# Performance work log

Hardware: AMD Instinct MI355X
Metric: run time of the kernel (lower is better)

The kernel has to match this reference:

```python
import jax, jax.numpy as jnp
import numpy as np

NUM_HEADS = 32
NUM_KV_HEADS = 8
HEAD_DIM = 128
HIDDEN = 4096
ROPE_THETA = 10000.0
SLIDING_WINDOW = 1024
NEG_INF = -1e9


def _make_sliding_window_mask(q_len, kv_len, window):
    # additive mask: 0 where attendable (causal AND within window), -inf otherwise
    i = jnp.arange(q_len)[:, None]
    j = jnp.arange(kv_len)[None, :]
    allowed = (j <= i) & (j > i - window)
    return jnp.where(allowed, 0.0, NEG_INF).astype(jnp.float32)[None, None]  # [1,1,q,kv]


def _rope_tables(seq_len, head_dim, theta):
    inv_freq = 1.0 / (theta ** (jnp.arange(0, head_dim, 2, dtype=jnp.float32) / head_dim))
    t = jnp.arange(seq_len, dtype=jnp.float32)
    freqs = jnp.einsum('i,j->ij', t, inv_freq)        # [S, D/2]
    emb = jnp.concatenate([freqs, freqs], axis=-1)     # [S, D]
    return jnp.cos(emb), jnp.sin(emb)


def _rotate_half(x):
    d = x.shape[-1] // 2
    return jnp.concatenate([-x[..., d:], x[..., :d]], axis=-1)


def setup_inputs() -> dict:
    key = jax.random.key(0)
    ks = jax.random.split(key, 5)
    B, S = 1, 2048
    sc = 0.02
    hidden_states = jax.random.normal(ks[0], (B, S, HIDDEN), dtype=jnp.float32)
    Wq = jax.random.normal(ks[1], (HIDDEN, NUM_HEADS * HEAD_DIM), dtype=jnp.float32) * sc
    Wk = jax.random.normal(ks[2], (HIDDEN, NUM_KV_HEADS * HEAD_DIM), dtype=jnp.float32) * sc
    Wv = jax.random.normal(ks[3], (HIDDEN, NUM_KV_HEADS * HEAD_DIM), dtype=jnp.float32) * sc
    Wo = jax.random.normal(ks[4], (NUM_HEADS * HEAD_DIM, HIDDEN), dtype=jnp.float32) * sc
    attention_mask = _make_sliding_window_mask(S, S, SLIDING_WINDOW)
    position_ids = jnp.arange(S, dtype=jnp.int64)[None, :]
    return {"hidden_states": hidden_states, "attention_mask": attention_mask,
            "position_ids": position_ids, "Wq": Wq, "Wk": Wk, "Wv": Wv, "Wo": Wo}


def reference(hidden_states, attention_mask, position_ids, Wq, Wk, Wv, Wo):
    B, S, _ = hidden_states.shape
    # projections
    q = (hidden_states @ Wq).reshape(B, S, NUM_HEADS, HEAD_DIM).transpose(0, 2, 1, 3)      # [B,H,S,D]
    k = (hidden_states @ Wk).reshape(B, S, NUM_KV_HEADS, HEAD_DIM).transpose(0, 2, 1, 3)   # [B,Hk,S,D]
    v = (hidden_states @ Wv).reshape(B, S, NUM_KV_HEADS, HEAD_DIM).transpose(0, 2, 1, 3)
    # RoPE
    cos_t, sin_t = _rope_tables(S, HEAD_DIM, ROPE_THETA)
    cos = cos_t[position_ids][:, None]  # [B,1,S,D]
    sin = sin_t[position_ids][:, None]
    q = q * cos + _rotate_half(q) * sin
    k = k * cos + _rotate_half(k) * sin
    # repeat_kv (GQA): [B,Hk,S,D] -> [B,H,S,D]
    n_rep = NUM_HEADS // NUM_KV_HEADS
    k = jnp.repeat(k, n_rep, axis=1)
    v = jnp.repeat(v, n_rep, axis=1)
    # attention
    scores = jnp.einsum('bhqd,bhkd->bhqk', q, k) / np.sqrt(HEAD_DIM)
    scores = scores + attention_mask
    probs = jax.nn.softmax(scores, axis=-1)
    out = jnp.einsum('bhqk,bhkd->bhqd', probs, v)
    out = out.transpose(0, 2, 1, 3).reshape(B, S, HIDDEN)
    return out @ Wo
```

## Files before the change

### kernel.cpp

```cpp
#include <hip/hip_runtime.h>

typedef __attribute__((ext_vector_type(8))) short short8;
typedef __attribute__((ext_vector_type(4))) short s16x4;
typedef __attribute__((ext_vector_type(4))) float f32x4;
typedef unsigned short u16;
typedef unsigned int u32;

__device__ __forceinline__ u16 f2bf(float f) {
  union { float f; unsigned int u; } v; v.f = f;
  unsigned int r = (v.u + 0x7FFFu + ((v.u >> 16) & 1u)) >> 16;
  return (u16)r;
}
__device__ __forceinline__ float bf2f(u16 b) {
  union { unsigned int u; float f; } v; v.u = ((unsigned int)b) << 16;
  return v.f;
}
__device__ __forceinline__ void load_lds16(const void* g, void* l) {
  __builtin_amdgcn_global_load_lds((const __attribute__((address_space(1))) void*)g,
                                   (__attribute__((address_space(3))) void*)l, 16, 0, 0);
}

__global__ void cvt_f32_bf16_kernel(const float* __restrict__ in, u16* __restrict__ out, int n4) {
  int i = blockIdx.x * blockDim.x + threadIdx.x;
  if (i >= n4) return;
  float4 v = ((const float4*)in)[i];
  ushort4 o;
  o.x = f2bf(v.x); o.y = f2bf(v.y); o.z = f2bf(v.z); o.w = f2bf(v.w);
  ((ushort4*)out)[i] = o;
}

__global__ void combine2_f32_kernel(float* __restrict__ out, const u16* __restrict__ p0,
                                    const u16* __restrict__ p1, int n8) {
  int i = blockIdx.x * blockDim.x + threadIdx.x;
  if (i >= n8) return;
  short8 a = ((const short8*)p0)[i];
  short8 b = ((const short8*)p1)[i];
  float4 o0, o1;
  o0.x = bf2f((u16)a[0]) + bf2f((u16)b[0]);
  o0.y = bf2f((u16)a[1]) + bf2f((u16)b[1]);
  o0.z = bf2f((u16)a[2]) + bf2f((u16)b[2]);
  o0.w = bf2f((u16)a[3]) + bf2f((u16)b[3]);
  o1.x = bf2f((u16)a[4]) + bf2f((u16)b[4]);
  o1.y = bf2f((u16)a[5]) + bf2f((u16)b[5]);
  o1.z = bf2f((u16)a[6]) + bf2f((u16)b[6]);
  o1.w = bf2f((u16)a[7]) + bf2f((u16)b[7]);
  ((float4*)out)[i * 2]     = o0;
  ((float4*)out)[i * 2 + 1] = o1;
}

__global__ void combine_kv_kernel(const u16* __restrict__ PKV, u16* __restrict__ Kb,
                                  u16* __restrict__ Vt) {
  int i = blockIdx.x * blockDim.x + threadIdx.x;
  const u16* src; u16* dst; size_t off;
  if (i < 262144) { off = (size_t)i; dst = Kb; src = PKV; }
  else            { off = (size_t)(i - 262144); dst = Vt; src = PKV + 2097152; }
  float s[8] = {0.f, 0.f, 0.f, 0.f, 0.f, 0.f, 0.f, 0.f};
#pragma unroll
  for (int z = 0; z < 4; ++z) {
    short8 v = *(const short8*)(src + (size_t)z * 4194304 + off * 8);
#pragma unroll
    for (int j = 0; j < 8; ++j) s[j] += bf2f((u16)v[j]);
  }
  short8 o;
#pragma unroll
  for (int j = 0; j < 8; ++j) o[j] = (short)f2bf(s[j]);
  ((short8*)dst)[off] = o;
}

__device__ __forceinline__ void tconv64_tile(const float* __restrict__ W, u16* __restrict__ Wt,
                                             int K, int N, int nb, int kb, int tid) {
  __shared__ float tile[64][65];
  int tx = tid & 15, ty = tid >> 4;
  const float* src = W + (size_t)(kb + ty) * N + nb + tx * 4;
#pragma unroll
  for (int i = 0; i < 4; ++i) {
    float4 v = *(const float4*)(src + (size_t)i * 16 * N);
    tile[ty + i * 16][tx * 4 + 0] = v.x;
    tile[ty + i * 16][tx * 4 + 1] = v.y;
    tile[ty + i * 16][tx * 4 + 2] = v.z;
    tile[ty + i * 16][tx * 4 + 3] = v.w;
  }
  __syncthreads();
  u16* dst = Wt + (size_t)(nb + ty) * K + kb + tx * 4;
#pragma unroll
  for (int i = 0; i < 4; ++i) {
    s16x4 o;
#pragma unroll
    for (int j = 0; j < 4; ++j) o[j] = (short)f2bf(tile[tx * 4 + j][ty + i * 16]);
    *(s16x4*)(dst + (size_t)i * 16 * K) = o;
  }
}

__global__ void tconv3_kernel(const float* __restrict__ Wq, const float* __restrict__ Wk,
                              const float* __restrict__ Wv, u16* __restrict__ WqT,
                              u16* __restrict__ WkvT) {
  int id = blockIdx.x;
  if (id < 4096)      tconv64_tile(Wq, WqT, 4096, 4096, (id & 63) * 64, (id >> 6) * 64, threadIdx.x);
  else if (id < 5120) { int t = id - 4096; tconv64_tile(Wk, WkvT, 4096, 1024, (t & 15) * 64, (t >> 4) * 64, threadIdx.x); }
  else                { int t = id - 5120; tconv64_tile(Wv, WkvT + (size_t)1024 * 4096, 4096, 1024, (t & 15) * 64, (t >> 4) * 64, threadIdx.x); }
}

__global__ void tconv1_kernel(const float* __restrict__ W, u16* __restrict__ Wt) {
  int id = blockIdx.x;
  tconv64_tile(W, Wt, 4096, 4096, (id & 63) * 64, (id >> 6) * 64, threadIdx.x);
}

__global__ void rope_kernel(u16* __restrict__ Qb, const u16* __restrict__ Qp1, u16* __restrict__ Kb) {
  int idx = blockIdx.x * blockDim.x + threadIdx.x;
  int j, t, hh, s;
  if (idx < 4194304) {
    j = idx & 63; t = idx >> 6; hh = t & 31; s = t >> 5;
    float invf = exp2f(-(float)j * (13.287712379549449f / 64.0f));
    float ang = (float)s * invf;
    float sn, cs;
    sincosf(ang, &sn, &cs);
    size_t base = (size_t)s * 4096 + hh * 128 + j;
    u16* p = Qb + base;
    const u16* p1 = Qp1 + base;
    float a = bf2f(p[0]) + bf2f(p1[0]);
    float b = bf2f(p[64]) + bf2f(p1[64]);
    const float scale = 0.12751781828987514f;
    p[0]  = f2bf((a * cs - b * sn) * scale);
    p[64] = f2bf((b * cs + a * sn) * scale);
  } else {
    int id = idx - 4194304;
    j = id & 63; t = id >> 6; hh = t & 7; s = t >> 3;
    float invf = exp2f(-(float)j * (13.287712379549449f / 64.0f));
    float ang = (float)s * invf;
    float sn, cs;
    sincosf(ang, &sn, &cs);
    u16* p = Kb + (size_t)s * 1024 + hh * 128 + j;
    float a = bf2f(p[0]), b = bf2f(p[64]);
    p[0]  = f2bf(a * cs - b * sn);
    p[64] = f2bf(b * cs + a * sn);
  }
}

__global__ __launch_bounds__(512, 1) void gemm256_kernel(
    const u16* __restrict__ A, const u16* __restrict__ B,
    u16* __restrict__ C0, u16* __restrict__ C1, int N, int K, int KH) {
  __shared__ u16 As[2][256 * 64];
  __shared__ u16 Bs[2][256 * 64];
  int tid = threadIdx.x, lane = tid & 63, wid = tid >> 6;
  int wr = wid >> 2, wc = wid & 3;
  int g = lane >> 4, q = lane & 15;
  int id = blockIdx.z * gridDim.x * gridDim.y + blockIdx.y * gridDim.x + blockIdx.x;
  int tot = gridDim.x * gridDim.y * gridDim.z;
  int swz = (id & 7) * (tot >> 3) + (id >> 3);
  int perh = gridDim.x * gridDim.y;
  int z = swz / perh, rem = swz % perh;
  int m0 = (rem / gridDim.x) * 256, n0 = (rem % gridDim.x) * 256;
  int k0 = z * KH;
  f32x4 acc[8][4];
#pragma unroll
  for (int i = 0; i < 8; ++i)
#pragma unroll
    for (int j = 0; j < 4; ++j) acc[i][j] = (f32x4){0.f, 0.f, 0.f, 0.f};
  int srow = tid >> 3;
  int scol = ((tid & 7) ^ (srow & 7)) << 3;
  const u16* ga = A + (size_t)(m0 + srow) * K + k0 + scol;
  const u16* gb = B + (size_t)(n0 + srow) * K + k0 + scol;
  int xorm = (q & 7) << 3;
  int arow = wr * 128 + q;
  int brow = wc * 64 + q;
  int nt = KH >> 6;

  auto stage = [&](int buf, int t) {
    const u16* pa = ga + t * 64;
    const u16* pb = gb + t * 64;
#pragma unroll
    for (int it = 0; it < 4; ++it) {
      load_lds16(pa + (size_t)it * 64 * K, (char*)(&As[buf][0]) + it * 8192 + tid * 16);
      load_lds16(pb + (size_t)it * 64 * K, (char*)(&Bs[buf][0]) + it * 8192 + tid * 16);
    }
  };

  stage(0, 0);
  stage(1, 1);
  asm volatile("s_waitcnt vmcnt(8)" ::: "memory");
  __builtin_amdgcn_s_barrier();
  for (int t = 0; t < nt; ++t) {
    int cur = t & 1;
    int col0 = (g * 8) ^ xorm;
    short8 a0[8], b0[4];
#pragma unroll
    for (int m = 0; m < 8; ++m) a0[m] = *(const short8*)&As[cur][(arow + m * 16) * 64 + col0];
#pragma unroll
    for (int n = 0; n < 4; ++n) b0[n] = *(const short8*)&Bs[cur][(brow + n * 16) * 64 + col0];
    __builtin_amdgcn_s_setprio(1);
#pragma unroll
    for (int m = 0; m < 8; ++m)
#pragma unroll
      for (int n = 0; n < 4; ++n)
        acc[m][n] = __builtin_amdgcn_mfma_f32_16x16x32_bf16(a0[m], b0[n], acc[m][n], 0, 0, 0);
    __builtin_amdgcn_s_setprio(0);
    int col1 = (32 + g * 8) ^ xorm;
    short8 a1[8], b1[4];
#pragma unroll
    for (int m = 0; m < 8; ++m) a1[m] = *(const short8*)&As[cur][(arow + m * 16) * 64 + col1];
#pragma unroll
    for (int n = 0; n < 4; ++n) b1[n] = *(const short8*)&Bs[cur][(brow + n * 16) * 64 + col1];
    asm volatile("s_waitcnt lgkmcnt(0)" ::: "memory");
    __builtin_amdgcn_s_barrier();
    if (t + 2 < nt) stage(cur, t + 2);
    __builtin_amdgcn_sched_barrier(0);
    __builtin_amdgcn_s_setprio(1);
#pragma unroll
    for (int m = 0; m < 8; ++m)
#pragma unroll
      for (int n = 0; n < 4; ++n)
        acc[m][n] = __builtin_amdgcn_mfma_f32_16x16x32_bf16(a1[m], b1[n], acc[m][n], 0, 0, 0);
    __builtin_amdgcn_s_setprio(0);
    if (t + 2 < nt)      { asm volatile("s_waitcnt vmcnt(8)" ::: "memory"); }
    else if (t + 1 < nt) { asm volatile("s_waitcnt vmcnt(0)" ::: "memory"); }
    __builtin_amdgcn_s_barrier();
  }
  int crow = m0 + wr * 128 + g * 4;
  int ccol = n0 + wc * 64 + q;
  u16* dst = z ? C1 : C0;
#pragma unroll
  for (int fm = 0; fm < 8; ++fm)
#pragma unroll
    for (int fn = 0; fn < 4; ++fn)
#pragma unroll
      for (int r = 0; r < 4; ++r)
        dst[(size_t)(crow + fm * 16 + r) * N + ccol + fn * 16] = f2bf(acc[fm][fn][r]);
}

__global__ __launch_bounds__(512, 1) void gemm_kv256_kernel(
    const u16* __restrict__ A, const u16* __restrict__ B,
    u16* __restrict__ PKV, int K, int KH) {
  __shared__ u16 As[2][256 * 64];
  __shared__ u16 Bs[2][256 * 64];
  int tid = threadIdx.x, lane = tid & 63, wid = tid >> 6;
  int wr = wid >> 2, wc = wid & 3;
  int g = lane >> 4, q = lane & 15;
  int id = blockIdx.z * 64 + blockIdx.y * 8 + blockIdx.x;
  int swz = (id & 7) * 32 + (id >> 3);
  int z = swz >> 6, rem = swz & 63;
  int m0 = (rem >> 3) * 256, n0 = (rem & 7) * 256;
  int k0 = z * KH;
  f32x4 acc[8][4];
#pragma unroll
  for (int i = 0; i < 8; ++i)
#pragma unroll
    for (int j = 0; j < 4; ++j) acc[i][j] = (f32x4){0.f, 0.f, 0.f, 0.f};
  int srow = tid >> 3;
  int scol = ((tid & 7) ^ (srow & 7)) << 3;
  const u16* ga = A + (size_t)(m0 + srow) * K + k0 + scol;
  const u16* gb = B + (size_t)(n0 + srow) * K + k0 + scol;
  int xorm = (q & 7) << 3;
  int arow = wr * 128 + q;
  int brow = wc * 64 + q;
  int nt = KH >> 6;

  auto stage = [&](int buf, int t) {
    const u16* pa = ga + t * 64;
    const u16* pb = gb + t * 64;
#pragma unroll
    for (int it = 0; it < 4; ++it) {
      load_lds16(pa + (size_t)it * 64 * K, (char*)(&As[buf][0]) + it * 8192 + tid * 16);
      load_lds16(pb + (size_t)it * 64 * K, (char*)(&Bs[buf][0]) + it * 8192 + tid * 16);
    }
  };

  stage(0, 0);
  stage(1, 1);
  asm volatile("s_waitcnt vmcnt(8)" ::: "memory");
  __builtin_amdgcn_s_barrier();
  for (int t = 0; t < nt; ++t) {
    int cur = t & 1;
    int col0 = (g * 8) ^ xorm;
    short8 a0[8], b0[4];
#pragma unroll
    for (int m = 0; m < 8; ++m) a0[m] = *(const short8*)&As[cur][(arow + m * 16) * 64 + col0];
#pragma unroll
    for (int n = 0; n < 4; ++n) b0[n] = *(const short8*)&Bs[cur][(brow + n * 16) * 64 + col0];
    __builtin_amdgcn_s_setprio(1);
#pragma unroll
    for (int m = 0; m < 8; ++m)
#pragma unroll
      for (int n = 0; n < 4; ++n)
        acc[m][n] = __builtin_amdgcn_mfma_f32_16x16x32_bf16(a0[m], b0[n], acc[m][n], 0, 0, 0);
    __builtin_amdgcn_s_setprio(0);
    int col1 = (32 + g * 8) ^ xorm;
    short8 a1[8], b1[4];
#pragma unroll
    for (int m = 0; m < 8; ++m) a1[m] = *(const short8*)&As[cur][(arow + m * 16) * 64 + col1];
#pragma unroll
    for (int n = 0; n < 4; ++n) b1[n] = *(const short8*)&Bs[cur][(brow + n * 16) * 64 + col1];
    asm volatile("s_waitcnt lgkmcnt(0)" ::: "memory");
    __builtin_amdgcn_s_barrier();
    if (t + 2 < nt) stage(cur, t + 2);
    __builtin_amdgcn_sched_barrier(0);
    __builtin_amdgcn_s_setprio(1);
#pragma unroll
    for (int m = 0; m < 8; ++m)
#pragma unroll
      for (int n = 0; n < 4; ++n)
        acc[m][n] = __builtin_amdgcn_mfma_f32_16x16x32_bf16(a1[m], b1[n], acc[m][n], 0, 0, 0);
    __builtin_amdgcn_s_setprio(0);
    if (t + 2 < nt)      { asm volatile("s_waitcnt vmcnt(8)" ::: "memory"); }
    else if (t + 1 < nt) { asm volatile("s_waitcnt vmcnt(0)" ::: "memory"); }
    __builtin_amdgcn_s_barrier();
  }
  int crow = m0 + wr * 128 + g * 4;
  int ccol = n0 + wc * 64 + q;
  u16* Kpart = PKV + (size_t)z * 4194304;
  u16* Vpart = Kpart + 2097152;
  if (n0 < 1024) {
#pragma unroll
    for (int fm = 0; fm < 8; ++fm)
#pragma unroll
      for (int fn = 0; fn < 4; ++fn)
#pragma unroll
        for (int r = 0; r < 4; ++r)
          Kpart[(size_t)(crow + fm * 16 + r) * 1024 + ccol + fn * 16] = f2bf(acc[fm][fn][r]);
  } else {
#pragma unroll
    for (int fn = 0; fn < 4; ++fn) {
      int vcol = ccol + fn * 16 - 1024;
#pragma unroll
      for (int fm = 0; fm < 8; ++fm) {
        s16x4 o;
#pragma unroll
        for (int r = 0; r < 4; ++r) o[r] = (short)f2bf(acc[fm][fn][r]);
        *(s16x4*)(Vpart + (size_t)vcol * 2048 + crow + fm * 16) = o;
      }
    }
  }
}

__global__ __launch_bounds__(512, 4) void attn_kernel(
    const u16* __restrict__ Q, const u16* __restrict__ Kg,
    const u16* __restrict__ Vt, u16* __restrict__ O) {
  __shared__ u16 Ks[2][64 * 128];
  __shared__ u16 Vs[2][128 * 64];
  int tid = threadIdx.x, lane = tid & 63, w = tid >> 6;
  int wg = w >> 2;
  int g = lane >> 4, q = lane & 15;
  int q0 = blockIdx.x * 128;
  int h = blockIdx.y, hk = h >> 2;
  int qbase = q0 + wg * 64;
  int qrow = qbase + (w & 3) * 16;
  int xorm = (lane & 7) << 3;
  short8 qf[4];
  {
    const u16* qp = Q + (size_t)(qrow + q) * 4096 + h * 128 + g * 8;
#pragma unroll
    for (int kk = 0; kk < 4; ++kk) qf[kk] = *(const short8*)(qp + kk * 32);
  }
  float mrow = -1e30f, lsum = 0.f;
  f32x4 of[8];
#pragma unroll
  for (int d = 0; d < 8; ++d) of[d] = (f32x4){0.f, 0.f, 0.f, 0.f};
  int bjt_lo = (q0 >= 1024) ? ((q0 - 1023) >> 6) : 0;
  int bjt_hi = (q0 + 64) >> 6;
  int wjt_lo = (qbase >= 1024) ? ((qbase - 1023) >> 6) : 0;
  int wjt_hi = qbase >> 6;
  int krow = tid >> 4;
  int kchunk = (tid & 15) ^ (krow & 7);
  const u16* kbase = Kg + (size_t)krow * 1024 + hk * 128 + (kchunk << 3);
  int vrow = tid >> 3;
  int vchunk = (tid & 7) ^ (vrow & 7);
  const u16* vbase = Vt + (size_t)(hk * 128 + vrow) * 2048 + (vchunk << 3);

  auto stageK = [&](int buf, int j0) {
    const u16* gp = kbase + (size_t)j0 * 1024;
#pragma unroll
    for (int it = 0; it < 2; ++it)
      load_lds16(gp + (size_t)it * 32 * 1024, (char*)(&Ks[buf][0]) + it * 8192 + tid * 16);
  };
  auto stageV = [&](int buf, int j0) {
    const u16* gp = vbase + j0;
#pragma unroll
    for (int it = 0; it < 2; ++it)
      load_lds16(gp + (size_t)it * 64 * 2048, (char*)(&Vs[buf][0]) + it * 8192 + tid * 16);
  };

  int cur = 0;
  stageK(0, bjt_lo << 6);
  stageV(0, bjt_lo << 6);
  asm volatile("s_waitcnt vmcnt(0)" ::: "memory");
  __syncthreads();
  for (int jt = bjt_lo; jt <= bjt_hi; ++jt) {
    int j0 = jt << 6;
    if (jt < bjt_hi) { stageK(cur ^ 1, j0 + 64); stageV(cur ^ 1, j0 + 64); }
    if (jt >= wjt_lo && jt <= wjt_hi) {
      f32x4 sf[4];
#pragma unroll
      for (int nt = 0; nt < 4; ++nt) sf[nt] = (f32x4){0.f, 0.f, 0.f, 0.f};
      const u16* ks = &Ks[cur][0];
      __builtin_amdgcn_s_setprio(1);
#pragma unroll
      for (int kk = 0; kk < 4; ++kk) {
        short8 qv = qf[kk];
        int col = (kk * 32 + g * 8) ^ xorm;
#pragma unroll
        for (int nt = 0; nt < 4; ++nt) {
          short8 kf = *(const short8*)&ks[(nt * 16 + q) * 128 + col];
          sf[nt] = __builtin_amdgcn_mfma_f32_16x16x32_bf16(kf, qv, sf[nt], 0, 0, 0);
        }
      }
      __builtin_amdgcn_s_setprio(0);
      float p[4][4];
#pragma unroll
      for (int nt = 0; nt < 4; ++nt)
#pragma unroll
        for (int r = 0; r < 4; ++r) p[nt][r] = sf[nt][r];
      if (j0 + 63 > qrow || j0 + 1009 <= qrow) {
        int qq = qrow + q;
        int kb = j0 + g * 4;
#pragma unroll
        for (int nt = 0; nt < 4; ++nt)
#pragma unroll
          for (int r = 0; r < 4; ++r) {
            int key = kb + nt * 16 + r;
            if (key > qq || key + 1024 <= qq) p[nt][r] = -1e9f;
          }
      }
      float tm = p[0][0];
#pragma unroll
      for (int nt = 0; nt < 4; ++nt)
#pragma unroll
        for (int r = 0; r < 4; ++r) tm = fmaxf(tm, p[nt][r]);
      tm = fmaxf(tm, __shfl_xor(tm, 16));
      tm = fmaxf(tm, __shfl_xor(tm, 32));
      if (__any(tm > mrow + 8.f)) {
        float nm = fmaxf(mrow, tm);
        float sc = __builtin_amdgcn_exp2f(mrow - nm);
        mrow = nm;
        lsum *= sc;
#pragma unroll
        for (int d = 0; d < 8; ++d) of[d] *= sc;
      }
      float ps = 0.f;
#pragma unroll
      for (int nt = 0; nt < 4; ++nt)
#pragma unroll
        for (int r = 0; r < 4; ++r) {
          float e = __builtin_amdgcn_exp2f(p[nt][r] - mrow);
          p[nt][r] = e;
          ps += e;
        }
      ps += __shfl_xor(ps, 16);
      ps += __shfl_xor(ps, 32);
      lsum += ps;
      u32 pk[4][2];
#pragma unroll
      for (int nt = 0; nt < 4; ++nt) {
        pk[nt][0] = __builtin_amdgcn_perm(__float_as_uint(p[nt][1]), __float_as_uint(p[nt][0]), 0x07060302u);
        pk[nt][1] = __builtin_amdgcn_perm(__float_as_uint(p[nt][3]), __float_as_uint(p[nt][2]), 0x07060302u);
      }
      int s0 = q + ((g & 1) ? 32 : 0);
      int s1 = s0 + 16;
      bool hi_sel = g >= 2;
      const u16* vs = &Vs[cur][0];
      __builtin_amdgcn_s_setprio(1);
#pragma unroll
      for (int kh = 0; kh < 2; ++kh) {
        int lo = kh * 2, hi = lo + 1;
        u32 a0 = (u32)__shfl((int)pk[lo][0], s0);
        u32 a1 = (u32)__shfl((int)pk[lo][1], s0);
        u32 b0 = (u32)__shfl((int)pk[hi][0], s0);
        u32 b1 = (u32)__shfl((int)pk[hi][1], s0);
        u32 a2 = (u32)__shfl((int)pk[lo][0], s1);
        u32 a3 = (u32)__shfl((int)pk[lo][1], s1);
        u32 b2 = (u32)__shfl((int)pk[hi][0], s1);
        u32 b3 = (u32)__shfl((int)pk[hi][1], s1);
        union { u32 u[4]; short8 s; } pb;
        pb.u[0] = hi_sel ? b0 : a0;
        pb.u[1] = hi_sel ? b1 : a1;
        pb.u[2] = hi_sel ? b2 : a2;
        pb.u[3] = hi_sel ? b3 : a3;
        int col = (kh * 32 + g * 8) ^ xorm;
#pragma unroll
        for (int dt = 0; dt < 8; ++dt) {
          short8 vv = *(const short8*)&vs[(dt * 16 + q) * 64 + col];
          of[dt] = __builtin_amdgcn_mfma_f32_16x16x32_bf16(vv, pb.s, of[dt], 0, 0, 0);
        }
      }
      __builtin_amdgcn_s_setprio(0);
    }
    asm volatile("s_waitcnt vmcnt(0)" ::: "memory");
    __builtin_amdgcn_s_barrier();
    cur ^= 1;
  }
  float inv = 1.f / lsum;
  u16* op = O + (size_t)(qrow + q) * 4096 + h * 128 + g * 4;
#pragma unroll
  for (int dt = 0; dt < 8; ++dt) {
    s16x4 o4;
#pragma unroll
    for (int r = 0; r < 4; ++r) o4[r] = (short)f2bf(of[dt][r] * inv);
    *(s16x4*)(op + dt * 16) = o4;
  }
}

extern "C" void kernel_launch(void* const* d_in, const int* in_sizes, int n_in,
                              void* d_out, int out_size, void* d_ws, size_t ws_size,
                              hipStream_t stream) {
  (void)in_sizes; (void)n_in; (void)out_size;
  const float* hs = (const float*)d_in[0];
  const float* Wq = (const float*)d_in[3];
  const float* Wk = (const float*)d_in[4];
  const float* Wv = (const float*)d_in[5];
  const float* Wo = (const float*)d_in[6];
  float* out = (float*)d_out;
  char* ws = (char*)d_ws;

  u16* Xb   = (u16*)(ws + 0);
  u16* Wt   = (u16*)(ws + 16777216);
  u16* WkvT = (u16*)(ws + 50331648);
  u16* Qb   = (u16*)(ws + 67108864);
  u16* Kb   = (u16*)(ws + 83886080);
  u16* Vtb  = (u16*)(ws + 88080384);
  u16* Ab   = (u16*)(ws + 96468992);
  u16* P1q  = Ab;
  u16* PKV  = Wt;
  u16* P0o  = WkvT;
  u16* P1o  = Qb;
  if (ws_size < 113246208u) return;

  cvt_f32_bf16_kernel<<<dim3(2097152 / 256), 256, 0, stream>>>(hs, Xb, 2097152);

  tconv3_kernel<<<dim3(6144), 256, 0, stream>>>(Wq, Wk, Wv, Wt, WkvT);

  gemm256_kernel<<<dim3(16, 8, 2), 512, 0, stream>>>(Xb, Wt, Qb, P1q, 4096, 4096, 2048);

  gemm_kv256_kernel<<<dim3(8, 8, 4), 512, 0, stream>>>(Xb, WkvT, PKV, 4096, 1024);
  combine_kv_kernel<<<dim3(2048), 256, 0, stream>>>(PKV, Kb, Vtb);

  rope_kernel<<<dim3(20480), 256, 0, stream>>>(Qb, P1q, Kb);

  attn_kernel<<<dim3(16, 32), 512, 0, stream>>>(Qb, Kb, Vtb, Ab);

  tconv1_kernel<<<dim3(4096), 256, 0, stream>>>(Wo, Wt);
  gemm256_kernel<<<dim3(16, 8, 2), 512, 0, stream>>>(Ab, Wt, P0o, P1o, 4096, 4096, 2048);
  combine2_f32_kernel<<<dim3(4096), 256, 0, stream>>>(out, P0o, P1o, 1048576);
}
```

Measured before the change: 311.7 us.

## Restructure GEMM mainloop into eight-phase half-tile pipeline with finer staging

Replaces the two-phase double-buffered GEMM loop with an eight-phase schedule that splits each 64-wide K tile into two 32-wide halves per matrix, interleaving global-to-LDS loads of the half tiles with smaller MFMA groups separated by barriers. The Q/O and KV GEMMs are unified into one templated kernel with an epilogue switch. The aim is to overlap memory traffic with compute more finely and cut register pressure by holding only 4 A fragments at a time. In exchange it adds more barriers per tile and drops the XOR swizzle, so the 64-byte-stride LDS reads may hit bank conflicts.

```diff
diff --git a/kernel.cpp b/kernel.cpp
--- a/kernel.cpp
+++ b/kernel.cpp
@@ -136,11 +136,11 @@
   }
 }
 
-__global__ __launch_bounds__(512, 1) void gemm256_kernel(
+template<int KVEPI>
+__global__ __launch_bounds__(512, 1) void gemm8p_kernel(
     const u16* __restrict__ A, const u16* __restrict__ B,
     u16* __restrict__ C0, u16* __restrict__ C1, int N, int K, int KH) {
-  __shared__ u16 As[2][256 * 64];
-  __shared__ u16 Bs[2][256 * 64];
+  __shared__ u16 Sh[2][2][2][8192];
   int tid = threadIdx.x, lane = tid & 63, wid = tid >> 6;
   int wr = wid >> 2, wc = wid & 3;
   int g = lane >> 4, q = lane & 15;
@@ -156,178 +156,120 @@
   for (int i = 0; i < 8; ++i)
 #pragma unroll
     for (int j = 0; j < 4; ++j) acc[i][j] = (f32x4){0.f, 0.f, 0.f, 0.f};
-  int srow = tid >> 3;
-  int scol = ((tid & 7) ^ (srow & 7)) << 3;
+  int srow = tid >> 2;
+  int scol = (tid & 3) * 8;
   const u16* ga = A + (size_t)(m0 + srow) * K + k0 + scol;
   const u16* gb = B + (size_t)(n0 + srow) * K + k0 + scol;
-  int xorm = (q & 7) << 3;
   int arow = wr * 128 + q;
   int brow = wc * 64 + q;
   int nt = KH >> 6;
 
-  auto stage = [&](int buf, int t) {
-    const u16* pa = ga + t * 64;
-    const u16* pb = gb + t * 64;
-#pragma unroll
-    for (int it = 0; it < 4; ++it) {
-      load_lds16(pa + (size_t)it * 64 * K, (char*)(&As[buf][0]) + it * 8192 + tid * 16);
-      load_lds16(pb + (size_t)it * 64 * K, (char*)(&Bs[buf][0]) + it * 8192 + tid * 16);
-    }
+  auto stageH = [&](int b, int mat, int h, int t) {
+    const u16* gp = (mat ? gb : ga) + t * 64 + h * 32;
+    char* dst = (char*)&Sh[b][mat][h][0];
+#pragma unroll
+    for (int it = 0; it < 2; ++it)
+      load_lds16(gp + (size_t)it * 128 * K, dst + it * 8192 + tid * 16);
   };
-
-  stage(0, 0);
-  stage(1, 1);
-  asm volatile("s_waitcnt vmcnt(8)" ::: "memory");
+  auto readA = [&](int b, int h, int fb, short8 (&af)[4]) {
+    const u16* s = &Sh[b][0][h][0];
+#pragma unroll
+    for (int m = 0; m < 4; ++m)
+      af[m] = *(const short8*)&s[(arow + (fb + m) * 16) * 32 + g * 8];
+  };
+  auto readB = [&](int b, int h, short8 (&bf)[4]) {
+    const u16* s = &Sh[b][1][h][0];
+#pragma unroll
+    for (int n = 0; n < 4; ++n)
+      bf[n] = *(const short8*)&s[(brow + n * 16) * 32 + g * 8];
+  };
+
+  stageH(0, 0, 0, 0); stageH(0, 1, 0, 0);
+  stageH(0, 0, 1, 0); stageH(0, 1, 1, 0);
+  stageH(1, 0, 0, 1); stageH(1, 1, 0, 1);
+  asm volatile("s_waitcnt vmcnt(4)" ::: "memory");
   __builtin_amdgcn_s_barrier();
-  for (int t = 0; t < nt; ++t) {
-    int cur = t & 1;
-    int col0 = (g * 8) ^ xorm;
-    short8 a0[8], b0[4];
-#pragma unroll
-    for (int m = 0; m < 8; ++m) a0[m] = *(const short8*)&As[cur][(arow + m * 16) * 64 + col0];
-#pragma unroll
-    for (int n = 0; n < 4; ++n) b0[n] = *(const short8*)&Bs[cur][(brow + n * 16) * 64 + col0];
-    __builtin_amdgcn_s_setprio(1);
-#pragma unroll
-    for (int m = 0; m < 8; ++m)
-#pragma unroll
-      for (int n = 0; n < 4; ++n)
-        acc[m][n] = __builtin_amdgcn_mfma_f32_16x16x32_bf16(a0[m], b0[n], acc[m][n], 0, 0, 0);
-    __builtin_amdgcn_s_setprio(0);
-    int col1 = (32 + g * 8) ^ xorm;
-    short8 a1[8], b1[4];
-#pragma unroll
-    for (int m = 0; m < 8; ++m) a1[m] = *(const short8*)&As[cur][(arow + m * 16) * 64 + col1];
-#pragma unroll
-    for (int n = 0; n < 4; ++n) b1[n] = *(const short8*)&Bs[cur][(brow + n * 16) * 64 + col1];
-    asm volatile("s_waitcnt lgkmcnt(0)" ::: "memory");
-    __builtin_amdgcn_s_barrier();
-    if (t + 2 < nt) stage(cur, t + 2);
-    __builtin_amdgcn_sched_barrier(0);
-    __builtin_amdgcn_s_setprio(1);
-#pragma unroll
-    for (int m = 0; m < 8; ++m)
-#pragma unroll
-      for (int n = 0; n < 4; ++n)
-        acc[m][n] = __builtin_amdgcn_mfma_f32_16x16x32_bf16(a1[m], b1[n], acc[m][n], 0, 0, 0);
-    __builtin_amdgcn_s_setprio(0);
-    if (t + 2 < nt)      { asm volatile("s_waitcnt vmcnt(8)" ::: "memory"); }
-    else if (t + 1 < nt) { asm volatile("s_waitcnt vmcnt(0)" ::: "memory"); }
-    __builtin_amdgcn_s_barrier();
-  }
+
+#define PHASE(FB)                                                        \
+  __builtin_amdgcn_s_barrier();                                          \
+  asm volatile("s_waitcnt lgkmcnt(0)" ::: "memory");                     \
+  __builtin_amdgcn_sched_barrier(0);                                     \
+  __builtin_amdgcn_s_setprio(1);                                         \
+  _Pragma("unroll")                                                      \
+  for (int m = 0; m < 4; ++m)                                            \
+    _Pragma("unroll")                                                    \
+    for (int n = 0; n < 4; ++n)                                          \
+      acc[FB + m][n] = __builtin_amdgcn_mfma_f32_16x16x32_bf16(          \
+          af[m], bf[n], acc[FB + m][n], 0, 0, 0);                        \
+  __builtin_amdgcn_s_setprio(0);                                         \
+  __builtin_amdgcn_s_barrier();
+
+  for (int t = 0; t < nt; t += 2) {
+    bool s2 = (t + 2 < nt);
+    short8 af[4], bf[4];
+    readA(0, 0, 0, af); readB(0, 0, bf);
+    stageH(1, 0, 1, t + 1);
+    PHASE(0)
+    readA(0, 0, 4, af);
+    stageH(1, 1, 1, t + 1);
+    PHASE(4)
+    readA(0, 1, 0, af); readB(0, 1, bf);
+    if (s2) stageH(0, 0, 0, t + 2);
+    PHASE(0)
+    readA(0, 1, 4, af);
+    if (s2) stageH(0, 1, 0, t + 2);
+    PHASE(4)
+    readA(1, 0, 0, af); readB(1, 0, bf);
+    if (s2) { stageH(0, 0, 1, t + 2); asm volatile("s_waitcnt vmcnt(6)" ::: "memory"); }
+    else    { asm volatile("s_waitcnt vmcnt(0)" ::: "memory"); }
+    PHASE(0)
+    readA(1, 0, 4, af);
+    if (s2) stageH(0, 1, 1, t + 2);
+    PHASE(4)
+    readA(1, 1, 0, af); readB(1, 1, bf);
+    if (s2) stageH(1, 0, 0, t + 3);
+    PHASE(0)
+    readA(1, 1, 4, af);
+    if (s2) { stageH(1, 1, 0, t + 3); asm volatile("s_waitcnt vmcnt(4)" ::: "memory"); }
+    PHASE(4)
+  }
+#undef PHASE
+
   int crow = m0 + wr * 128 + g * 4;
   int ccol = n0 + wc * 64 + q;
-  u16* dst = z ? C1 : C0;
-#pragma unroll
-  for (int fm = 0; fm < 8; ++fm)
-#pragma unroll
-    for (int fn = 0; fn < 4; ++fn)
-#pragma unroll
-      for (int r = 0; r < 4; ++r)
-        dst[(size_t)(crow + fm * 16 + r) * N + ccol + fn * 16] = f2bf(acc[fm][fn][r]);
-}
-
-__global__ __launch_bounds__(512, 1) void gemm_kv256_kernel(
-    const u16* __restrict__ A, const u16* __restrict__ B,
-    u16* __restrict__ PKV, int K, int KH) {
-  __shared__ u16 As[2][256 * 64];
-  __shared__ u16 Bs[2][256 * 64];
-  int tid = threadIdx.x, lane = tid & 63, wid = tid >> 6;
-  int wr = wid >> 2, wc = wid & 3;
-  int g = lane >> 4, q = lane & 15;
-  int id = blockIdx.z * 64 + blockIdx.y * 8 + blockIdx.x;
-  int swz = (id & 7) * 32 + (id >> 3);
-  int z = swz >> 6, rem = swz & 63;
-  int m0 = (rem >> 3) * 256, n0 = (rem & 7) * 256;
-  int k0 = z * KH;
-  f32x4 acc[8][4];
-#pragma unroll
-  for (int i = 0; i < 8; ++i)
-#pragma unroll
-    for (int j = 0; j < 4; ++j) acc[i][j] = (f32x4){0.f, 0.f, 0.f, 0.f};
-  int srow = tid >> 3;
-  int scol = ((tid & 7) ^ (srow & 7)) << 3;
-  const u16* ga = A + (size_t)(m0 + srow) * K + k0 + scol;
-  const u16* gb = B + (size_t)(n0 + srow) * K + k0 + scol;
-  int xorm = (q & 7) << 3;
-  int arow = wr * 128 + q;
-  int brow = wc * 64 + q;
-  int nt = KH >> 6;
-
-  auto stage = [&](int buf, int t) {
-    const u16* pa = ga + t * 64;
-    const u16* pb = gb + t * 64;
-#pragma unroll
-    for (int it = 0; it < 4; ++it) {
-      load_lds16(pa + (size_t)it * 64 * K, (char*)(&As[buf][0]) + it * 8192 + tid * 16);
-      load_lds16(pb + (size_t)it * 64 * K, (char*)(&Bs[buf][0]) + it * 8192 + tid * 16);
+  if (KVEPI) {
+    u16* Kpart = C0 + (size_t)z * 4194304;
+    u16* Vpart = Kpart + 2097152;
+    if (n0 < 1024) {
+#pragma unroll
+      for (int fm = 0; fm < 8; ++fm)
+#pragma unroll
+        for (int fn = 0; fn < 4; ++fn)
+#pragma unroll
+          for (int r = 0; r < 4; ++r)
+            Kpart[(size_t)(crow + fm * 16 + r) * 1024 + ccol + fn * 16] = f2bf(acc[fm][fn][r]);
+    } else {
+#pragma unroll
+      for (int fn = 0; fn < 4; ++fn) {
+        int vcol = ccol + fn * 16 - 1024;
+#pragma unroll
+        for (int fm = 0; fm < 8; ++fm) {
+          s16x4 o;
+#pragma unroll
+          for (int r = 0; r < 4; ++r) o[r] = (short)f2bf(acc[fm][fn][r]);
+          *(s16x4*)(Vpart + (size_t)vcol * 2048 + crow + fm * 16) = o;
+        }
+      }
     }
-  };
-
-  stage(0, 0);
-  stage(1, 1);
-  asm volatile("s_waitcnt vmcnt(8)" ::: "memory");
-  __builtin_amdgcn_s_barrier();
-  for (int t = 0; t < nt; ++t) {
-    int cur = t & 1;
-    int col0 = (g * 8) ^ xorm;
-    short8 a0[8], b0[4];
-#pragma unroll
-    for (int m = 0; m < 8; ++m) a0[m] = *(const short8*)&As[cur][(arow + m * 16) * 64 + col0];
-#pragma unroll
-    for (int n = 0; n < 4; ++n) b0[n] = *(const short8*)&Bs[cur][(brow + n * 16) * 64 + col0];
-    __builtin_amdgcn_s_setprio(1);
-#pragma unroll
-    for (int m = 0; m < 8; ++m)
-#pragma unroll
-      for (int n = 0; n < 4; ++n)
-        acc[m][n] = __builtin_amdgcn_mfma_f32_16x16x32_bf16(a0[m], b0[n], acc[m][n], 0, 0, 0);
-    __builtin_amdgcn_s_setprio(0);
-    int col1 = (32 + g * 8) ^ xorm;
-    short8 a1[8], b1[4];
-#pragma unroll
-    for (int m = 0; m < 8; ++m) a1[m] = *(const short8*)&As[cur][(arow + m * 16) * 64 + col1];
-#pragma unroll
-    for (int n = 0; n < 4; ++n) b1[n] = *(const short8*)&Bs[cur][(brow + n * 16) * 64 + col1];
-    asm volatile("s_waitcnt lgkmcnt(0)" ::: "memory");
-    __builtin_amdgcn_s_barrier();
-    if (t + 2 < nt) stage(cur, t + 2);
-    __builtin_amdgcn_sched_barrier(0);
-    __builtin_amdgcn_s_setprio(1);
-#pragma unroll
-    for (int m = 0; m < 8; ++m)
-#pragma unroll
-      for (int n = 0; n < 4; ++n)
-        acc[m][n] = __builtin_amdgcn_mfma_f32_16x16x32_bf16(a1[m], b1[n], acc[m][n], 0, 0, 0);
-    __builtin_amdgcn_s_setprio(0);
-    if (t + 2 < nt)      { asm volatile("s_waitcnt vmcnt(8)" ::: "memory"); }
-    else if (t + 1 < nt) { asm volatile("s_waitcnt vmcnt(0)" ::: "memory"); }
-    __builtin_amdgcn_s_barrier();
-  }
-  int crow = m0 + wr * 128 + g * 4;
-  int ccol = n0 + wc * 64 + q;
-  u16* Kpart = PKV + (size_t)z * 4194304;
-  u16* Vpart = Kpart + 2097152;
-  if (n0 < 1024) {
+  } else {
+    u16* dst = z ? C1 : C0;
 #pragma unroll
     for (int fm = 0; fm < 8; ++fm)
 #pragma unroll
       for (int fn = 0; fn < 4; ++fn)
 #pragma unroll
         for (int r = 0; r < 4; ++r)
-          Kpart[(size_t)(crow + fm * 16 + r) * 1024 + ccol + fn * 16] = f2bf(acc[fm][fn][r]);
-  } else {
-#pragma unroll
-    for (int fn = 0; fn < 4; ++fn) {
-      int vcol = ccol + fn * 16 - 1024;
-#pragma unroll
-      for (int fm = 0; fm < 8; ++fm) {
-        s16x4 o;
-#pragma unroll
-        for (int r = 0; r < 4; ++r) o[r] = (short)f2bf(acc[fm][fn][r]);
-        *(s16x4*)(Vpart + (size_t)vcol * 2048 + crow + fm * 16) = o;
-      }
-    }
+          dst[(size_t)(crow + fm * 16 + r) * N + ccol + fn * 16] = f2bf(acc[fm][fn][r]);
   }
 }
 
@@ -526,9 +468,9 @@
 
   tconv3_kernel<<<dim3(6144), 256, 0, stream>>>(Wq, Wk, Wv, Wt, WkvT);
 
-  gemm256_kernel<<<dim3(16, 8, 2), 512, 0, stream>>>(Xb, Wt, Qb, P1q, 4096, 4096, 2048);
-
-  gemm_kv256_kernel<<<dim3(8, 8, 4), 512, 0, stream>>>(Xb, WkvT, PKV, 4096, 1024);
+  gemm8p_kernel<0><<<dim3(16, 8, 2), 512, 0, stream>>>(Xb, Wt, Qb, P1q, 4096, 4096, 2048);
+
+  gemm8p_kernel<1><<<dim3(8, 8, 4), 512, 0, stream>>>(Xb, WkvT, PKV, nullptr, 2048, 4096, 1024);
   combine_kv_kernel<<<dim3(2048), 256, 0, stream>>>(PKV, Kb, Vtb);
 
   rope_kernel<<<dim3(20480), 256, 0, stream>>>(Qb, P1q, Kb);
@@ -536,6 +478,6 @@
   attn_kernel<<<dim3(16, 32), 512, 0, stream>>>(Qb, Kb, Vtb, Ab);
 
   tconv1_kernel<<<dim3(4096), 256, 0, stream>>>(Wo, Wt);
-  gemm256_kernel<<<dim3(16, 8, 2), 512, 0, stream>>>(Ab, Wt, P0o, P1o, 4096, 4096, 2048);
+  gemm8p_kernel<0><<<dim3(16, 8, 2), 512, 0, stream>>>(Ab, Wt, P0o, P1o, 4096, 4096, 2048);
   combine2_f32_kernel<<<dim3(4096), 256, 0, stream>>>(out, P0o, P1o, 1048576);
 }
```

Result: slower. 326.6 us (+4.8%).

## Fuse RoPE into KV combine and attention Q load, drop rope kernel

Applied to the files above, without the earlier changes.

Removes the standalone RoPE kernel. K rotation now happens inside the split-K combine kernel, and Q's two split-K partials are summed, rotated and scaled when the attention kernel loads Q fragments. This saves one full read-modify-write pass over Q and K plus a launch. The cost is that attention reads two Q buffers and does sincos work per block, and the attention output buffer is moved onto Xb.

```diff
diff --git a/kernel.cpp b/kernel.cpp
--- a/kernel.cpp
+++ b/kernel.cpp
@@ -48,23 +48,48 @@
   ((float4*)out)[i * 2 + 1] = o1;
 }
 
-__global__ void combine_kv_kernel(const u16* __restrict__ PKV, u16* __restrict__ Kb,
-                                  u16* __restrict__ Vt) {
+__global__ void combine_kv_rope_kernel(const u16* __restrict__ PKV, u16* __restrict__ Kb,
+                                       u16* __restrict__ Vt) {
   int i = blockIdx.x * blockDim.x + threadIdx.x;
-  const u16* src; u16* dst; size_t off;
-  if (i < 262144) { off = (size_t)i; dst = Kb; src = PKV; }
-  else            { off = (size_t)(i - 262144); dst = Vt; src = PKV + 2097152; }
-  float s[8] = {0.f, 0.f, 0.f, 0.f, 0.f, 0.f, 0.f, 0.f};
-#pragma unroll
-  for (int z = 0; z < 4; ++z) {
-    short8 v = *(const short8*)(src + (size_t)z * 4194304 + off * 8);
-#pragma unroll
-    for (int j = 0; j < 8; ++j) s[j] += bf2f((u16)v[j]);
-  }
-  short8 o;
-#pragma unroll
-  for (int j = 0; j < 8; ++j) o[j] = (short)f2bf(s[j]);
-  ((short8*)dst)[off] = o;
+  if (i < 131072) {
+    int s = i >> 6, r = i & 63, hh = r >> 3, c = r & 7;
+    size_t lo8 = (size_t)s * 128 + hh * 16 + c;
+    size_t hi8 = lo8 + 8;
+    float lo[8] = {0,0,0,0,0,0,0,0}, hi[8] = {0,0,0,0,0,0,0,0};
+#pragma unroll
+    for (int z = 0; z < 4; ++z) {
+      short8 a = *(const short8*)(PKV + (size_t)z * 4194304 + lo8 * 8);
+      short8 b = *(const short8*)(PKV + (size_t)z * 4194304 + hi8 * 8);
+#pragma unroll
+      for (int j = 0; j < 8; ++j) { lo[j] += bf2f((u16)a[j]); hi[j] += bf2f((u16)b[j]); }
+    }
+    short8 olo, ohi;
+#pragma unroll
+    for (int ii = 0; ii < 8; ++ii) {
+      int j = c * 8 + ii;
+      float invf = exp2f(-(float)j * (13.287712379549449f / 64.0f));
+      float sn, cs;
+      sincosf((float)s * invf, &sn, &cs);
+      olo[ii] = (short)f2bf(lo[ii] * cs - hi[ii] * sn);
+      ohi[ii] = (short)f2bf(hi[ii] * cs + lo[ii] * sn);
+    }
+    *(short8*)(Kb + lo8 * 8) = olo;
+    *(short8*)(Kb + hi8 * 8) = ohi;
+  } else {
+    int v = i - 131072;
+    const u16* src = PKV + 2097152;
+    float sm[8] = {0,0,0,0,0,0,0,0};
+#pragma unroll
+    for (int z = 0; z < 4; ++z) {
+      short8 a = *(const short8*)(src + (size_t)z * 4194304 + (size_t)v * 8);
+#pragma unroll
+      for (int j = 0; j < 8; ++j) sm[j] += bf2f((u16)a[j]);
+    }
+    short8 o;
+#pragma unroll
+    for (int j = 0; j < 8; ++j) o[j] = (short)f2bf(sm[j]);
+    ((short8*)Vt)[v] = o;
+  }
 }
 
 __device__ __forceinline__ void tconv64_tile(const float* __restrict__ W, u16* __restrict__ Wt,
@@ -103,37 +128,6 @@
 __global__ void tconv1_kernel(const float* __restrict__ W, u16* __restrict__ Wt) {
   int id = blockIdx.x;
   tconv64_tile(W, Wt, 4096, 4096, (id & 63) * 64, (id >> 6) * 64, threadIdx.x);
-}
-
-__global__ void rope_kernel(u16* __restrict__ Qb, const u16* __restrict__ Qp1, u16* __restrict__ Kb) {
-  int idx = blockIdx.x * blockDim.x + threadIdx.x;
-  int j, t, hh, s;
-  if (idx < 4194304) {
-    j = idx & 63; t = idx >> 6; hh = t & 31; s = t >> 5;
-    float invf = exp2f(-(float)j * (13.287712379549449f / 64.0f));
-    float ang = (float)s * invf;
-    float sn, cs;
-    sincosf(ang, &sn, &cs);
-    size_t base = (size_t)s * 4096 + hh * 128 + j;
-    u16* p = Qb + base;
-    const u16* p1 = Qp1 + base;
-    float a = bf2f(p[0]) + bf2f(p1[0]);
-    float b = bf2f(p[64]) + bf2f(p1[64]);
-    const float scale = 0.12751781828987514f;
-    p[0]  = f2bf((a * cs - b * sn) * scale);
-    p[64] = f2bf((b * cs + a * sn) * scale);
-  } else {
-    int id = idx - 4194304;
-    j = id & 63; t = id >> 6; hh = t & 7; s = t >> 3;
-    float invf = exp2f(-(float)j * (13.287712379549449f / 64.0f));
-    float ang = (float)s * invf;
-    float sn, cs;
-    sincosf(ang, &sn, &cs);
-    u16* p = Kb + (size_t)s * 1024 + hh * 128 + j;
-    float a = bf2f(p[0]), b = bf2f(p[64]);
-    p[0]  = f2bf(a * cs - b * sn);
-    p[64] = f2bf(b * cs + a * sn);
-  }
 }
 
 __global__ __launch_bounds__(512, 1) void gemm256_kernel(
@@ -332,8 +326,8 @@
 }
 
 __global__ __launch_bounds__(512, 4) void attn_kernel(
-    const u16* __restrict__ Q, const u16* __restrict__ Kg,
-    const u16* __restrict__ Vt, u16* __restrict__ O) {
+    const u16* __restrict__ Q0, const u16* __restrict__ Q1,
+    const u16* __restrict__ Kg, const u16* __restrict__ Vt, u16* __restrict__ O) {
   __shared__ u16 Ks[2][64 * 128];
   __shared__ u16 Vs[2][128 * 64];
   int tid = threadIdx.x, lane = tid & 63, w = tid >> 6;
@@ -346,9 +340,29 @@
   int xorm = (lane & 7) << 3;
   short8 qf[4];
   {
-    const u16* qp = Q + (size_t)(qrow + q) * 4096 + h * 128 + g * 8;
-#pragma unroll
-    for (int kk = 0; kk < 4; ++kk) qf[kk] = *(const short8*)(qp + kk * 32);
+    size_t qoff = (size_t)(qrow + q) * 4096 + h * 128 + g * 8;
+    float sum[4][8];
+#pragma unroll
+    for (int kk = 0; kk < 4; ++kk) {
+      short8 a = *(const short8*)(Q0 + qoff + kk * 32);
+      short8 b = *(const short8*)(Q1 + qoff + kk * 32);
+#pragma unroll
+      for (int i = 0; i < 8; ++i) sum[kk][i] = bf2f((u16)a[i]) + bf2f((u16)b[i]);
+    }
+    const float scale = 0.12751781828987514f;
+    float srow = (float)(qrow + q);
+#pragma unroll
+    for (int kk = 0; kk < 2; ++kk)
+#pragma unroll
+      for (int i = 0; i < 8; ++i) {
+        int j = kk * 32 + g * 8 + i;
+        float invf = exp2f(-(float)j * (13.287712379549449f / 64.0f));
+        float sn, cs;
+        sincosf(srow * invf, &sn, &cs);
+        float lo = sum[kk][i], hi = sum[kk + 2][i];
+        qf[kk][i]     = (short)f2bf((lo * cs - hi * sn) * scale);
+        qf[kk + 2][i] = (short)f2bf((hi * cs + lo * sn) * scale);
+      }
   }
   float mrow = -1e30f, lsum = 0.f;
   f32x4 of[8];
@@ -515,11 +529,11 @@
   u16* Qb   = (u16*)(ws + 67108864);
   u16* Kb   = (u16*)(ws + 83886080);
   u16* Vtb  = (u16*)(ws + 88080384);
-  u16* Ab   = (u16*)(ws + 96468992);
-  u16* P1q  = Ab;
+  u16* P1q  = (u16*)(ws + 96468992);
   u16* PKV  = Wt;
   u16* P0o  = WkvT;
   u16* P1o  = Qb;
+  u16* Ao   = Xb;
   if (ws_size < 113246208u) return;
 
   cvt_f32_bf16_kernel<<<dim3(2097152 / 256), 256, 0, stream>>>(hs, Xb, 2097152);
@@ -529,13 +543,11 @@
   gemm256_kernel<<<dim3(16, 8, 2), 512, 0, stream>>>(Xb, Wt, Qb, P1q, 4096, 4096, 2048);
 
   gemm_kv256_kernel<<<dim3(8, 8, 4), 512, 0, stream>>>(Xb, WkvT, PKV, 4096, 1024);
-  combine_kv_kernel<<<dim3(2048), 256, 0, stream>>>(PKV, Kb, Vtb);
-
-  rope_kernel<<<dim3(20480), 256, 0, stream>>>(Qb, P1q, Kb);
-
-  attn_kernel<<<dim3(16, 32), 512, 0, stream>>>(Qb, Kb, Vtb, Ab);
+  combine_kv_rope_kernel<<<dim3(1536), 256, 0, stream>>>(PKV, Kb, Vtb);
+
+  attn_kernel<<<dim3(16, 32), 512, 0, stream>>>(Qb, P1q, Kb, Vtb, Ao);
 
   tconv1_kernel<<<dim3(4096), 256, 0, stream>>>(Wo, Wt);
-  gemm256_kernel<<<dim3(16, 8, 2), 512, 0, stream>>>(Ab, Wt, P0o, P1o, 4096, 4096, 2048);
+  gemm256_kernel<<<dim3(16, 8, 2), 512, 0, stream>>>(Ao, Wt, P0o, P1o, 4096, 4096, 2048);
   combine2_f32_kernel<<<dim3(4096), 256, 0, stream>>>(out, P0o, P1o, 1048576);
 }
```

New measurement: 303.8 us. 2.5% less time.
